# Kernel tuning notes

Measured on AMD Instinct MI355X. Metric: run time of the kernel, lower is better.

The kernel has to match this reference:

```python
import jax, jax.numpy as jnp
import numpy as np

B, S, H, I = 2, 2048, 4096, 11008  # batch, seq, hidden_size, intermediate_size (Llama-7B)


def setup_inputs() -> dict:
    key = jax.random.key(0)
    ks = jax.random.split(key, 11)
    # int8 activations and weights (SmoothQuant W8A8)
    hidden_states = jax.random.randint(ks[0], (B, S, H), -128, 128, dtype=jnp.int8)
    w_gate = jax.random.randint(ks[1], (I, H), -128, 128, dtype=jnp.int8)
    w_up = jax.random.randint(ks[2], (I, H), -128, 128, dtype=jnp.int8)
    w_down = jax.random.randint(ks[3], (H, I), -128, 128, dtype=jnp.int8)
    # dequant scales (alpha = input_scale * weight_scale), small positive
    gate_a = jax.random.uniform(ks[4], (1,), dtype=jnp.float32) * 1e-4 + 1e-5
    up_a = jax.random.uniform(ks[5], (1,), dtype=jnp.float32) * 1e-4 + 1e-5
    down_a = jax.random.uniform(ks[6], (1,), dtype=jnp.float32) * 1e-4 + 1e-5
    # fp32 biases
    gate_b = jax.random.normal(ks[7], (I,), dtype=jnp.float32) * 0.01
    up_b = jax.random.normal(ks[8], (I,), dtype=jnp.float32) * 0.01
    down_b = jax.random.normal(ks[9], (H,), dtype=jnp.float32) * 0.01
    # requantization scale for down_proj input
    down_scale = jax.random.uniform(ks[10], (1,), dtype=jnp.float32) * 0.05 + 0.01
    return {
        "hidden_states": hidden_states,
        "w_gate": w_gate, "w_up": w_up, "w_down": w_down,
        "gate_a": gate_a, "gate_b": gate_b,
        "up_a": up_a, "up_b": up_b,
        "down_a": down_a, "down_b": down_b,
        "down_scale": down_scale,
    }


def _i8_gemm(x_i8, w_i8):
    return jnp.einsum("bsk,nk->bsn", x_i8, w_i8, preferred_element_type=jnp.int32)


def reference(hidden_states, w_gate, w_up, w_down,
              gate_a, gate_b, up_a, up_b, down_a, down_b, down_scale):
    # gate_proj: W8A8 GEMM -> dequant (alpha) + fp32 bias -> fused SiLU
    g = _i8_gemm(hidden_states, w_gate).astype(jnp.float32) * gate_a[0] + gate_b
    gate_out = g * jax.nn.sigmoid(g)  # SiLU
    # up_proj: W8A8 GEMM -> dequant + fp32 bias
    up_out = _i8_gemm(hidden_states, w_up).astype(jnp.float32) * up_a[0] + up_b
    inter = gate_out * up_out
    # requantize to int8 for down_proj input
    q = jnp.clip(jnp.round(inter / down_scale[0]), -128, 127).astype(jnp.int8)
    # down_proj: W8A8 GEMM -> dequant + fp32 bias
    down_out = _i8_gemm(q, w_down).astype(jnp.float32) * down_a[0] + down_b
    return down_out  # [B, S, H] fp32
```

## Files before the change

kernel.cpp:

```cpp
#include <hip/hip_runtime.h>
#include <cstdint>


typedef int v4i  __attribute__((ext_vector_type(4)));
typedef int v16i __attribute__((ext_vector_type(16)));

typedef const void __attribute__((address_space(1)))* gas_ptr;
typedef void __attribute__((address_space(3)))* las_ptr;

static constexpr int M_TOT = 4096;
static constexpr int HDIM  = 4096;
static constexpr int IDIM  = 11008;

#define MFMA_I8(a, b, c) __builtin_amdgcn_mfma_i32_32x32x32_i8((a), (b), (c), 0, 0, 0)
#define BAR()        asm volatile("s_barrier" ::: "memory")
#define WAIT_VM(N)   asm volatile("s_waitcnt vmcnt(" #N ")" ::: "memory")
#define SETPRIO(P)   __builtin_amdgcn_s_setprio(P)

__device__ __forceinline__ void gload16(const int8_t* g, int8_t* l) {
  __builtin_amdgcn_global_load_lds((gas_ptr)g, (las_ptr)l, 16, 0, 0);
}

__device__ __forceinline__ v4i frag64(const int8_t* lds, int row, int c) {
  const int pair = row >> 1;
  const int slot = ((c << 1) | (row & 1)) ^ (pair & 7);
  return *(const v4i*)(lds + pair * 128 + slot * 16);
}

__device__ __forceinline__ void relmap64(int rel, int& row, int& col) {
  const int pair = rel >> 3;
  const int sl = (rel & 7) ^ (pair & 7);
  row = 2 * pair + (sl & 1);
  col = (sl >> 1) * 16;
}

__device__ __forceinline__ void pack16(const int* __restrict__ src,
                                       int8_t* __restrict__ dst, int t) {
  const int4* s = (const int4*)(src) + t * 4;
  int4 v0 = s[0], v1 = s[1], v2 = s[2], v3 = s[3];
  int p0 = (v0.x & 0xff) | ((v0.y & 0xff) << 8) | ((v0.z & 0xff) << 16) | (v0.w << 24);
  int p1 = (v1.x & 0xff) | ((v1.y & 0xff) << 8) | ((v1.z & 0xff) << 16) | (v1.w << 24);
  int p2 = (v2.x & 0xff) | ((v2.y & 0xff) << 8) | ((v2.z & 0xff) << 16) | (v2.w << 24);
  int p3 = (v3.x & 0xff) | ((v3.y & 0xff) << 8) | ((v3.z & 0xff) << 16) | (v3.w << 24);
  ((int4*)dst)[t] = make_int4(p0, p1, p2, p3);
}

static constexpr int CX = (M_TOT * HDIM) / 16;
static constexpr int CW = (IDIM * HDIM) / 16;
static constexpr int CTOT = CX + 3 * CW;

__global__ __launch_bounds__(256) void k_pack_all(
    const int* __restrict__ X32, const int* __restrict__ Wg32,
    const int* __restrict__ Wu32, const int* __restrict__ Wd32,
    int8_t* __restrict__ Xp, int8_t* __restrict__ Wgp,
    int8_t* __restrict__ Wup, int8_t* __restrict__ Wdp) {
  int t = blockIdx.x * blockDim.x + threadIdx.x;
  if (t >= CTOT) return;
  if (t < CX)               { pack16(X32,  Xp,  t); return; }
  t -= CX;
  if (t < CW)               { pack16(Wg32, Wgp, t); return; }
  t -= CW;
  if (t < CW)               { pack16(Wu32, Wup, t); return; }
  t -= CW;
  pack16(Wd32, Wdp, t);
}

__global__ __launch_bounds__(256, 2) void k_gateup(
    const int8_t* __restrict__ X,
    const int8_t* __restrict__ Wg,
    const int8_t* __restrict__ Wu,
    const float* __restrict__ gate_a, const float* __restrict__ gate_b,
    const float* __restrict__ up_a,   const float* __restrict__ up_b,
    const float* __restrict__ down_scale,
    int8_t* __restrict__ Q) {
  __shared__ __align__(16) int8_t lds8[3 * 24576];

  const int tid  = threadIdx.x;
  const int lane = tid & 63;
  const int wave = tid >> 6;
  const int wn   = wave;
  const int half = lane >> 5;
  const int ln31 = lane & 31;

  const int m0 = blockIdx.x * 128;
  const int n0 = blockIdx.y * 128;

  const int8_t* Ab = X  + (size_t)m0 * HDIM;
  const int8_t* Gb = Wg + (size_t)n0 * HDIM;
  const int8_t* Ub = Wu + (size_t)n0 * HDIM;

  int r0, c0, r1, c1;
  relmap64(tid,       r0, c0);
  relmap64(tid + 256, r1, c1);
  const size_t o0 = (size_t)r0 * HDIM + c0;
  const size_t o1 = (size_t)r1 * HDIM + c1;
  const int l0 = tid * 16;
  const int l1 = (tid + 256) * 16;

  v16i accG[4], accU[4];
#pragma unroll
  for (int i = 0; i < 4; ++i)
#pragma unroll
    for (int e = 0; e < 16; ++e) { accG[i][e] = 0; accU[i][e] = 0; }

  const int rB = wn * 32 + ln31;

#define GU_STAGE(rr, bb)                                        \
  {                                                             \
    int8_t* sb = &lds8[(bb) * 24576];                           \
    const size_t ks = (size_t)(rr) * 64;                        \
    gload16(Ab + ks + o0, sb + l0);                             \
    gload16(Ab + ks + o1, sb + l1);                             \
    gload16(Gb + ks + o0, sb + 8192 + l0);                      \
    gload16(Gb + ks + o1, sb + 8192 + l1);                      \
    gload16(Ub + ks + o0, sb + 16384 + l0);                     \
    gload16(Ub + ks + o1, sb + 16384 + l1);                     \
  }

  GU_STAGE(0, 0)
  GU_STAGE(1, 1)
  WAIT_VM(6);
  BAR();

  const int NT = HDIM / 64;
  int bc = 0;
  int bs = 2;
  for (int r = 0; r < NT; ++r) {
    if (r + 2 < NT) GU_STAGE(r + 2, bs)

    const int8_t* bufA = &lds8[bc * 24576];
    const int8_t* bufG = bufA + 8192;
    const int8_t* bufU = bufA + 16384;
    SETPRIO(1);
#pragma unroll
    for (int ks = 0; ks < 2; ++ks) {
      const int c = 2 * ks + half;
      v4i a0 = frag64(bufA, ln31,      c);
      v4i a1 = frag64(bufA, ln31 + 32, c);
      v4i a2 = frag64(bufA, ln31 + 64, c);
      v4i a3 = frag64(bufA, ln31 + 96, c);
      v4i gg = frag64(bufG, rB, c);
      v4i uu = frag64(bufU, rB, c);
      accG[0] = MFMA_I8(a0, gg, accG[0]);
      accU[0] = MFMA_I8(a0, uu, accU[0]);
      accG[1] = MFMA_I8(a1, gg, accG[1]);
      accU[1] = MFMA_I8(a1, uu, accU[1]);
      accG[2] = MFMA_I8(a2, gg, accG[2]);
      accU[2] = MFMA_I8(a2, uu, accU[2]);
      accG[3] = MFMA_I8(a3, gg, accG[3]);
      accU[3] = MFMA_I8(a3, uu, accU[3]);
    }
    SETPRIO(0);

    if (r + 2 < NT)      { WAIT_VM(6); }
    else if (r + 1 < NT) { WAIT_VM(0); }
    if (r + 1 < NT) BAR();

    bc = (bc == 2) ? 0 : bc + 1;
    bs = (bs == 2) ? 0 : bs + 1;
  }
#undef GU_STAGE

  const float ga = gate_a[0];
  const float ua = up_a[0];
  const float inv_ds = 1.0f / down_scale[0];
  const int n = n0 + wn * 32 + ln31;
  const float gb = gate_b[n];
  const float ub = up_b[n];

#pragma unroll
  for (int tm = 0; tm < 4; ++tm) {
#pragma unroll
    for (int r = 0; r < 16; ++r) {
      const int row_l = (r & 3) + 8 * (r >> 2) + 4 * half;
      const int m = m0 + tm * 32 + row_l;
      const float g = (float)accG[tm][r] * ga + gb;
      const float u = (float)accU[tm][r] * ua + ub;
      const float sg = g / (1.0f + __expf(-g));
      const float inter = sg * u;
      float qf = rintf(inter * inv_ds);
      qf = fminf(127.0f, fmaxf(-128.0f, qf));
      Q[(size_t)m * IDIM + n] = (int8_t)qf;
    }
  }
}

__global__ __launch_bounds__(256, 2) void k_down(
    const int8_t* __restrict__ Qm,
    const int8_t* __restrict__ Wd,
    const float* __restrict__ down_a, const float* __restrict__ down_b,
    float* __restrict__ Out) {
  __shared__ __align__(16) int8_t lds8[3 * 24576];

  const int tid  = threadIdx.x;
  const int lane = tid & 63;
  const int wave = tid >> 6;
  const int wn   = wave;
  const int half = lane >> 5;
  const int ln31 = lane & 31;

  const int m0 = blockIdx.x * 128;
  const int n0 = blockIdx.y * 256;

  const int8_t* Ab = Qm + (size_t)m0 * IDIM;
  const int8_t* Bb = Wd + (size_t)n0 * IDIM;

  int ra0, ca0, ra1, ca1;
  relmap64(tid,       ra0, ca0);
  relmap64(tid + 256, ra1, ca1);
  const size_t oa0 = (size_t)ra0 * IDIM + ca0;
  const size_t oa1 = (size_t)ra1 * IDIM + ca1;
  int rb0, cb0, rb1, cb1, rb2, cb2, rb3, cb3;
  relmap64(tid,       rb0, cb0);
  relmap64(tid + 256, rb1, cb1);
  relmap64(tid + 512, rb2, cb2);
  relmap64(tid + 768, rb3, cb3);
  const size_t ob0 = (size_t)rb0 * IDIM + cb0;
  const size_t ob1 = (size_t)rb1 * IDIM + cb1;
  const size_t ob2 = (size_t)rb2 * IDIM + cb2;
  const size_t ob3 = (size_t)rb3 * IDIM + cb3;
  const int l0 = tid * 16;
  const int l1 = (tid + 256) * 16;
  const int l2 = (tid + 512) * 16;
  const int l3 = (tid + 768) * 16;

  v16i acc[4][2];
#pragma unroll
  for (int i = 0; i < 4; ++i)
#pragma unroll
    for (int j = 0; j < 2; ++j)
#pragma unroll
      for (int e = 0; e < 16; ++e) acc[i][j][e] = 0;

  const int rB = wn * 64 + ln31;

#define DN_STAGE(rr, bb)                                        \
  {                                                             \
    int8_t* sb = &lds8[(bb) * 24576];                           \
    const size_t ks = (size_t)(rr) * 64;                        \
    gload16(Ab + ks + oa0, sb + l0);                            \
    gload16(Ab + ks + oa1, sb + l1);                            \
    gload16(Bb + ks + ob0, sb + 8192 + l0);                     \
    gload16(Bb + ks + ob1, sb + 8192 + l1);                     \
    gload16(Bb + ks + ob2, sb + 8192 + l2);                     \
    gload16(Bb + ks + ob3, sb + 8192 + l3);                     \
  }

  DN_STAGE(0, 0)
  DN_STAGE(1, 1)
  WAIT_VM(6);
  BAR();

  const int NT = IDIM / 64;
  int bc = 0;
  int bs = 2;
  for (int r = 0; r < NT; ++r) {
    if (r + 2 < NT) DN_STAGE(r + 2, bs)

    const int8_t* bufA = &lds8[bc * 24576];
    const int8_t* bufB = bufA + 8192;
    SETPRIO(1);
#pragma unroll
    for (int ks = 0; ks < 2; ++ks) {
      const int c = 2 * ks + half;
      v4i a0 = frag64(bufA, ln31,      c);
      v4i a1 = frag64(bufA, ln31 + 32, c);
      v4i a2 = frag64(bufA, ln31 + 64, c);
      v4i a3 = frag64(bufA, ln31 + 96, c);
      v4i b0 = frag64(bufB, rB,      c);
      v4i b1 = frag64(bufB, rB + 32, c);
      acc[0][0] = MFMA_I8(a0, b0, acc[0][0]);
      acc[0][1] = MFMA_I8(a0, b1, acc[0][1]);
      acc[1][0] = MFMA_I8(a1, b0, acc[1][0]);
      acc[1][1] = MFMA_I8(a1, b1, acc[1][1]);
      acc[2][0] = MFMA_I8(a2, b0, acc[2][0]);
      acc[2][1] = MFMA_I8(a2, b1, acc[2][1]);
      acc[3][0] = MFMA_I8(a3, b0, acc[3][0]);
      acc[3][1] = MFMA_I8(a3, b1, acc[3][1]);
    }
    SETPRIO(0);

    if (r + 2 < NT)      { WAIT_VM(6); }
    else if (r + 1 < NT) { WAIT_VM(0); }
    if (r + 1 < NT) BAR();

    bc = (bc == 2) ? 0 : bc + 1;
    bs = (bs == 2) ? 0 : bs + 1;
  }
#undef DN_STAGE

  const float da = down_a[0];
#pragma unroll
  for (int tn = 0; tn < 2; ++tn) {
    const int n = n0 + wn * 64 + tn * 32 + ln31;
    const float db = down_b[n];
#pragma unroll
    for (int tm = 0; tm < 4; ++tm) {
#pragma unroll
      for (int r = 0; r < 16; ++r) {
        const int row_l = (r & 3) + 8 * (r >> 2) + 4 * half;
        const int m = m0 + tm * 32 + row_l;
        Out[(size_t)m * HDIM + n] = (float)acc[tm][tn][r] * da + db;
      }
    }
  }
}

extern "C" void kernel_launch(void* const* d_in, const int* in_sizes, int n_in,
                              void* d_out, int out_size, void* d_ws, size_t ws_size,
                              hipStream_t stream) {
  const int* X32        = (const int*)d_in[0];
  const int* Wg32       = (const int*)d_in[1];
  const int* Wu32       = (const int*)d_in[2];
  const int* Wd32       = (const int*)d_in[3];
  const float* gate_a   = (const float*)d_in[4];
  const float* gate_b   = (const float*)d_in[5];
  const float* up_a     = (const float*)d_in[6];
  const float* up_b     = (const float*)d_in[7];
  const float* down_a   = (const float*)d_in[8];
  const float* down_b   = (const float*)d_in[9];
  const float* down_scale = (const float*)d_in[10];
  float* Out = (float*)d_out;

  const size_t nX = (size_t)M_TOT * HDIM;
  const size_t nW = (size_t)IDIM * HDIM;

  int8_t* Q   = (int8_t*)d_ws;
  int8_t* Xp  = Q   + nW;
  int8_t* Wgp = Xp  + nX;
  int8_t* Wup = Wgp + nW;
  int8_t* Wdp = Wup + nW;

  k_pack_all<<<(CTOT + 255) / 256, 256, 0, stream>>>(X32, Wg32, Wu32, Wd32,
                                                     Xp, Wgp, Wup, Wdp);

  k_gateup<<<dim3(M_TOT / 128, IDIM / 128), dim3(256), 0, stream>>>(
      Xp, Wgp, Wup, gate_a, gate_b, up_a, up_b, down_scale, Q);

  k_down<<<dim3(M_TOT / 128, HDIM / 256), dim3(256), 0, stream>>>(
      Q, Wdp, down_a, down_b, Out);
}
```

Measured before the change: 1.143 ms.

## Load weight fragments directly to registers and stage only activations in LDS

Both GEMM kernels stop staging the weight tiles through LDS. Each lane now loads its B fragments straight from global memory into registers, double-buffered across iterations. Only the activation tile is staged in LDS, with the K step widened to 128 and three buffers kept. The aim is to cut LDS traffic and footprint, at the cost of uncoalesced 16-byte strided global loads per lane, more registers, and intricate vmcnt bookkeeping.

```diff
diff --git a/kernel.cpp b/kernel.cpp
--- a/kernel.cpp
+++ b/kernel.cpp
@@ -21,10 +21,11 @@
   __builtin_amdgcn_global_load_lds((gas_ptr)g, (las_ptr)l, 16, 0, 0);
 }
 
-__device__ __forceinline__ v4i frag64(const int8_t* lds, int row, int c) {
+__device__ __forceinline__ v4i fragA(const int8_t* buf, int row, int cg) {
   const int pair = row >> 1;
+  const int c    = cg & 3;
   const int slot = ((c << 1) | (row & 1)) ^ (pair & 7);
-  return *(const v4i*)(lds + pair * 128 + slot * 16);
+  return *(const v4i*)(buf + (cg >> 2) * 8192 + pair * 128 + slot * 16);
 }
 
 __device__ __forceinline__ void relmap64(int rel, int& row, int& col) {
@@ -33,6 +34,8 @@
   row = 2 * pair + (sl & 1);
   col = (sl >> 1) * 16;
 }
+
+__device__ __forceinline__ int inc3(int b) { return b == 2 ? 0 : b + 1; }
 
 __device__ __forceinline__ void pack16(const int* __restrict__ src,
                                        int8_t* __restrict__ dst, int t) {
@@ -65,6 +68,45 @@
   pack16(Wd32, Wdp, t);
 }
 
+__device__ __forceinline__ void stage_a(const int8_t* Ab, size_t ldk, int rr,
+                                        size_t o0, size_t o1, int l0, int l1,
+                                        int8_t* base) {
+  const int8_t* g = Ab + (size_t)rr * 128;
+  gload16(g + o0,      base + l0);
+  gload16(g + o1,      base + l1);
+  gload16(g + 64 + o0, base + 8192 + l0);
+  gload16(g + 64 + o1, base + 8192 + l1);
+  (void)ldk;
+}
+
+__device__ __forceinline__ void loadB_row(const int8_t* p, v4i (&b)[4]) {
+#pragma unroll
+  for (int i = 0; i < 4; ++i) b[i] = *(const v4i*)(p + i * 32);
+}
+
+__device__ __forceinline__ void gu_compute(const int8_t* buf, int ln31, int half,
+                                           const v4i (&bg)[4], const v4i (&bu)[4],
+                                           v16i (&accG)[4], v16i (&accU)[4]) {
+  SETPRIO(1);
+#pragma unroll
+  for (int ks = 0; ks < 4; ++ks) {
+    const int cg = 2 * ks + half;
+    v4i a0 = fragA(buf, ln31,      cg);
+    v4i a1 = fragA(buf, ln31 + 32, cg);
+    v4i a2 = fragA(buf, ln31 + 64, cg);
+    v4i a3 = fragA(buf, ln31 + 96, cg);
+    accG[0] = MFMA_I8(a0, bg[ks], accG[0]);
+    accU[0] = MFMA_I8(a0, bu[ks], accU[0]);
+    accG[1] = MFMA_I8(a1, bg[ks], accG[1]);
+    accU[1] = MFMA_I8(a1, bu[ks], accU[1]);
+    accG[2] = MFMA_I8(a2, bg[ks], accG[2]);
+    accU[2] = MFMA_I8(a2, bu[ks], accU[2]);
+    accG[3] = MFMA_I8(a3, bg[ks], accG[3]);
+    accU[3] = MFMA_I8(a3, bu[ks], accU[3]);
+  }
+  SETPRIO(0);
+}
+
 __global__ __launch_bounds__(256, 2) void k_gateup(
     const int8_t* __restrict__ X,
     const int8_t* __restrict__ Wg,
@@ -73,93 +115,83 @@
     const float* __restrict__ up_a,   const float* __restrict__ up_b,
     const float* __restrict__ down_scale,
     int8_t* __restrict__ Q) {
-  __shared__ __align__(16) int8_t lds8[3 * 24576];
+  __shared__ __align__(16) int8_t lds8[3 * 16384];
 
   const int tid  = threadIdx.x;
   const int lane = tid & 63;
-  const int wave = tid >> 6;
-  const int wn   = wave;
+  const int wn   = tid >> 6;
   const int half = lane >> 5;
   const int ln31 = lane & 31;
 
   const int m0 = blockIdx.x * 128;
   const int n0 = blockIdx.y * 128;
 
-  const int8_t* Ab = X  + (size_t)m0 * HDIM;
-  const int8_t* Gb = Wg + (size_t)n0 * HDIM;
-  const int8_t* Ub = Wu + (size_t)n0 * HDIM;
+  const int8_t* Ab = X + (size_t)m0 * HDIM;
 
   int r0, c0, r1, c1;
   relmap64(tid,       r0, c0);
   relmap64(tid + 256, r1, c1);
-  const size_t o0 = (size_t)r0 * HDIM + c0;
-  const size_t o1 = (size_t)r1 * HDIM + c1;
+  const size_t oA0 = (size_t)r0 * HDIM + c0;
+  const size_t oA1 = (size_t)r1 * HDIM + c1;
   const int l0 = tid * 16;
   const int l1 = (tid + 256) * 16;
 
+  const int n_lane = n0 + wn * 32 + ln31;
+  const int8_t* Gp = Wg + (size_t)n_lane * HDIM + half * 16;
+  const int8_t* Up = Wu + (size_t)n_lane * HDIM + half * 16;
+
   v16i accG[4], accU[4];
 #pragma unroll
   for (int i = 0; i < 4; ++i)
 #pragma unroll
     for (int e = 0; e < 16; ++e) { accG[i][e] = 0; accU[i][e] = 0; }
 
-  const int rB = wn * 32 + ln31;
-
-#define GU_STAGE(rr, bb)                                        \
-  {                                                             \
-    int8_t* sb = &lds8[(bb) * 24576];                           \
-    const size_t ks = (size_t)(rr) * 64;                        \
-    gload16(Ab + ks + o0, sb + l0);                             \
-    gload16(Ab + ks + o1, sb + l1);                             \
-    gload16(Gb + ks + o0, sb + 8192 + l0);                      \
-    gload16(Gb + ks + o1, sb + 8192 + l1);                      \
-    gload16(Ub + ks + o0, sb + 16384 + l0);                     \
-    gload16(Ub + ks + o1, sb + 16384 + l1);                     \
-  }
-
-  GU_STAGE(0, 0)
-  GU_STAGE(1, 1)
-  WAIT_VM(6);
+  v4i bG0[4], bU0[4], bG1[4], bU1[4];
+
+  const int NT = HDIM / 128;
+
+  stage_a(Ab, HDIM, 0, oA0, oA1, l0, l1, lds8);
+  stage_a(Ab, HDIM, 1, oA0, oA1, l0, l1, lds8 + 16384);
+  loadB_row(Gp, bG0);
+  loadB_row(Up, bU0);
+  WAIT_VM(12);
   BAR();
 
-  const int NT = HDIM / 64;
-  int bc = 0;
-  int bs = 2;
-  for (int r = 0; r < NT; ++r) {
-    if (r + 2 < NT) GU_STAGE(r + 2, bs)
-
-    const int8_t* bufA = &lds8[bc * 24576];
-    const int8_t* bufG = bufA + 8192;
-    const int8_t* bufU = bufA + 16384;
-    SETPRIO(1);
-#pragma unroll
-    for (int ks = 0; ks < 2; ++ks) {
-      const int c = 2 * ks + half;
-      v4i a0 = frag64(bufA, ln31,      c);
-      v4i a1 = frag64(bufA, ln31 + 32, c);
-      v4i a2 = frag64(bufA, ln31 + 64, c);
-      v4i a3 = frag64(bufA, ln31 + 96, c);
-      v4i gg = frag64(bufG, rB, c);
-      v4i uu = frag64(bufU, rB, c);
-      accG[0] = MFMA_I8(a0, gg, accG[0]);
-      accU[0] = MFMA_I8(a0, uu, accU[0]);
-      accG[1] = MFMA_I8(a1, gg, accG[1]);
-      accU[1] = MFMA_I8(a1, uu, accU[1]);
-      accG[2] = MFMA_I8(a2, gg, accG[2]);
-      accU[2] = MFMA_I8(a2, uu, accU[2]);
-      accG[3] = MFMA_I8(a3, gg, accG[3]);
-      accU[3] = MFMA_I8(a3, uu, accU[3]);
-    }
-    SETPRIO(0);
-
-    if (r + 2 < NT)      { WAIT_VM(6); }
-    else if (r + 1 < NT) { WAIT_VM(0); }
-    if (r + 1 < NT) BAR();
-
-    bc = (bc == 2) ? 0 : bc + 1;
-    bs = (bs == 2) ? 0 : bs + 1;
-  }
-#undef GU_STAGE
+  int bcur = 0;
+  for (int r = 0; r < NT; r += 2) {
+    {
+      if (r + 1 < NT) {
+        loadB_row(Gp + (size_t)(r + 1) * 128, bG1);
+        loadB_row(Up + (size_t)(r + 1) * 128, bU1);
+      }
+      if (r + 2 < NT) {
+        const int bst = inc3(inc3(bcur));
+        stage_a(Ab, HDIM, r + 2, oA0, oA1, l0, l1, lds8 + bst * 16384);
+      }
+      gu_compute(lds8 + bcur * 16384, ln31, half, bG0, bU0, accG, accU);
+      if (r + 1 < NT) {
+        if (r + 2 < NT) { WAIT_VM(12); } else { WAIT_VM(8); }
+        BAR();
+      }
+      bcur = inc3(bcur);
+    }
+    {
+      if (r + 2 < NT) {
+        loadB_row(Gp + (size_t)(r + 2) * 128, bG0);
+        loadB_row(Up + (size_t)(r + 2) * 128, bU0);
+      }
+      if (r + 3 < NT) {
+        const int bst = inc3(inc3(bcur));
+        stage_a(Ab, HDIM, r + 3, oA0, oA1, l0, l1, lds8 + bst * 16384);
+      }
+      gu_compute(lds8 + bcur * 16384, ln31, half, bG1, bU1, accG, accU);
+      if (r + 2 < NT) {
+        if (r + 3 < NT) { WAIT_VM(12); } else { WAIT_VM(8); }
+        BAR();
+      }
+      bcur = inc3(bcur);
+    }
+  }
 
   const float ga = gate_a[0];
   const float ua = up_a[0];
@@ -171,11 +203,11 @@
 #pragma unroll
   for (int tm = 0; tm < 4; ++tm) {
 #pragma unroll
-    for (int r = 0; r < 16; ++r) {
-      const int row_l = (r & 3) + 8 * (r >> 2) + 4 * half;
+    for (int e = 0; e < 16; ++e) {
+      const int row_l = (e & 3) + 8 * (e >> 2) + 4 * half;
       const int m = m0 + tm * 32 + row_l;
-      const float g = (float)accG[tm][r] * ga + gb;
-      const float u = (float)accU[tm][r] * ua + ub;
+      const float g = (float)accG[tm][e] * ga + gb;
+      const float u = (float)accU[tm][e] * ua + ub;
       const float sg = g / (1.0f + __expf(-g));
       const float inter = sg * u;
       float qf = rintf(inter * inv_ds);
@@ -185,17 +217,39 @@
   }
 }
 
+__device__ __forceinline__ void dn_compute(const int8_t* buf, int ln31, int half,
+                                           const v4i (&b0)[4], const v4i (&b1)[4],
+                                           v16i (&acc)[4][2]) {
+  SETPRIO(1);
+#pragma unroll
+  for (int ks = 0; ks < 4; ++ks) {
+    const int cg = 2 * ks + half;
+    v4i a0 = fragA(buf, ln31,      cg);
+    v4i a1 = fragA(buf, ln31 + 32, cg);
+    v4i a2 = fragA(buf, ln31 + 64, cg);
+    v4i a3 = fragA(buf, ln31 + 96, cg);
+    acc[0][0] = MFMA_I8(a0, b0[ks], acc[0][0]);
+    acc[0][1] = MFMA_I8(a0, b1[ks], acc[0][1]);
+    acc[1][0] = MFMA_I8(a1, b0[ks], acc[1][0]);
+    acc[1][1] = MFMA_I8(a1, b1[ks], acc[1][1]);
+    acc[2][0] = MFMA_I8(a2, b0[ks], acc[2][0]);
+    acc[2][1] = MFMA_I8(a2, b1[ks], acc[2][1]);
+    acc[3][0] = MFMA_I8(a3, b0[ks], acc[3][0]);
+    acc[3][1] = MFMA_I8(a3, b1[ks], acc[3][1]);
+  }
+  SETPRIO(0);
+}
+
 __global__ __launch_bounds__(256, 2) void k_down(
     const int8_t* __restrict__ Qm,
     const int8_t* __restrict__ Wd,
     const float* __restrict__ down_a, const float* __restrict__ down_b,
     float* __restrict__ Out) {
-  __shared__ __align__(16) int8_t lds8[3 * 24576];
+  __shared__ __align__(16) int8_t lds8[3 * 16384];
 
   const int tid  = threadIdx.x;
   const int lane = tid & 63;
-  const int wave = tid >> 6;
-  const int wn   = wave;
+  const int wn   = tid >> 6;
   const int half = lane >> 5;
   const int ln31 = lane & 31;
 
@@ -203,26 +257,18 @@
   const int n0 = blockIdx.y * 256;
 
   const int8_t* Ab = Qm + (size_t)m0 * IDIM;
-  const int8_t* Bb = Wd + (size_t)n0 * IDIM;
-
-  int ra0, ca0, ra1, ca1;
-  relmap64(tid,       ra0, ca0);
-  relmap64(tid + 256, ra1, ca1);
-  const size_t oa0 = (size_t)ra0 * IDIM + ca0;
-  const size_t oa1 = (size_t)ra1 * IDIM + ca1;
-  int rb0, cb0, rb1, cb1, rb2, cb2, rb3, cb3;
-  relmap64(tid,       rb0, cb0);
-  relmap64(tid + 256, rb1, cb1);
-  relmap64(tid + 512, rb2, cb2);
-  relmap64(tid + 768, rb3, cb3);
-  const size_t ob0 = (size_t)rb0 * IDIM + cb0;
-  const size_t ob1 = (size_t)rb1 * IDIM + cb1;
-  const size_t ob2 = (size_t)rb2 * IDIM + cb2;
-  const size_t ob3 = (size_t)rb3 * IDIM + cb3;
+
+  int r0, c0, r1, c1;
+  relmap64(tid,       r0, c0);
+  relmap64(tid + 256, r1, c1);
+  const size_t oA0 = (size_t)r0 * IDIM + c0;
+  const size_t oA1 = (size_t)r1 * IDIM + c1;
   const int l0 = tid * 16;
   const int l1 = (tid + 256) * 16;
-  const int l2 = (tid + 512) * 16;
-  const int l3 = (tid + 768) * 16;
+
+  const int n_row0 = n0 + wn * 64 + ln31;
+  const int8_t* B0p = Wd + (size_t)n_row0 * IDIM + half * 16;
+  const int8_t* B1p = B0p + (size_t)32 * IDIM;
 
   v16i acc[4][2];
 #pragma unroll
@@ -232,62 +278,52 @@
 #pragma unroll
       for (int e = 0; e < 16; ++e) acc[i][j][e] = 0;
 
-  const int rB = wn * 64 + ln31;
-
-#define DN_STAGE(rr, bb)                                        \
-  {                                                             \
-    int8_t* sb = &lds8[(bb) * 24576];                           \
-    const size_t ks = (size_t)(rr) * 64;                        \
-    gload16(Ab + ks + oa0, sb + l0);                            \
-    gload16(Ab + ks + oa1, sb + l1);                            \
-    gload16(Bb + ks + ob0, sb + 8192 + l0);                     \
-    gload16(Bb + ks + ob1, sb + 8192 + l1);                     \
-    gload16(Bb + ks + ob2, sb + 8192 + l2);                     \
-    gload16(Bb + ks + ob3, sb + 8192 + l3);                     \
-  }
-
-  DN_STAGE(0, 0)
-  DN_STAGE(1, 1)
-  WAIT_VM(6);
+  v4i bA0[4], bB0[4], bA1[4], bB1[4];
+
+  const int NT = IDIM / 128;
+
+  stage_a(Ab, IDIM, 0, oA0, oA1, l0, l1, lds8);
+  stage_a(Ab, IDIM, 1, oA0, oA1, l0, l1, lds8 + 16384);
+  loadB_row(B0p, bA0);
+  loadB_row(B1p, bB0);
+  WAIT_VM(12);
   BAR();
 
-  const int NT = IDIM / 64;
-  int bc = 0;
-  int bs = 2;
-  for (int r = 0; r < NT; ++r) {
-    if (r + 2 < NT) DN_STAGE(r + 2, bs)
-
-    const int8_t* bufA = &lds8[bc * 24576];
-    const int8_t* bufB = bufA + 8192;
-    SETPRIO(1);
-#pragma unroll
-    for (int ks = 0; ks < 2; ++ks) {
-      const int c = 2 * ks + half;
-      v4i a0 = frag64(bufA, ln31,      c);
-      v4i a1 = frag64(bufA, ln31 + 32, c);
-      v4i a2 = frag64(bufA, ln31 + 64, c);
-      v4i a3 = frag64(bufA, ln31 + 96, c);
-      v4i b0 = frag64(bufB, rB,      c);
-      v4i b1 = frag64(bufB, rB + 32, c);
-      acc[0][0] = MFMA_I8(a0, b0, acc[0][0]);
-      acc[0][1] = MFMA_I8(a0, b1, acc[0][1]);
-      acc[1][0] = MFMA_I8(a1, b0, acc[1][0]);
-      acc[1][1] = MFMA_I8(a1, b1, acc[1][1]);
-      acc[2][0] = MFMA_I8(a2, b0, acc[2][0]);
-      acc[2][1] = MFMA_I8(a2, b1, acc[2][1]);
-      acc[3][0] = MFMA_I8(a3, b0, acc[3][0]);
-      acc[3][1] = MFMA_I8(a3, b1, acc[3][1]);
-    }
-    SETPRIO(0);
-
-    if (r + 2 < NT)      { WAIT_VM(6); }
-    else if (r + 1 < NT) { WAIT_VM(0); }
-    if (r + 1 < NT) BAR();
-
-    bc = (bc == 2) ? 0 : bc + 1;
-    bs = (bs == 2) ? 0 : bs + 1;
-  }
-#undef DN_STAGE
+  int bcur = 0;
+  for (int r = 0; r < NT; r += 2) {
+    {
+      if (r + 1 < NT) {
+        loadB_row(B0p + (size_t)(r + 1) * 128, bA1);
+        loadB_row(B1p + (size_t)(r + 1) * 128, bB1);
+      }
+      if (r + 2 < NT) {
+        const int bst = inc3(inc3(bcur));
+        stage_a(Ab, IDIM, r + 2, oA0, oA1, l0, l1, lds8 + bst * 16384);
+      }
+      dn_compute(lds8 + bcur * 16384, ln31, half, bA0, bB0, acc);
+      if (r + 1 < NT) {
+        if (r + 2 < NT) { WAIT_VM(12); } else { WAIT_VM(8); }
+        BAR();
+      }
+      bcur = inc3(bcur);
+    }
+    {
+      if (r + 2 < NT) {
+        loadB_row(B0p + (size_t)(r + 2) * 128, bA0);
+        loadB_row(B1p + (size_t)(r + 2) * 128, bB0);
+      }
+      if (r + 3 < NT) {
+        const int bst = inc3(inc3(bcur));
+        stage_a(Ab, IDIM, r + 3, oA0, oA1, l0, l1, lds8 + bst * 16384);
+      }
+      dn_compute(lds8 + bcur * 16384, ln31, half, bA1, bB1, acc);
+      if (r + 2 < NT) {
+        if (r + 3 < NT) { WAIT_VM(12); } else { WAIT_VM(8); }
+        BAR();
+      }
+      bcur = inc3(bcur);
+    }
+  }
 
   const float da = down_a[0];
 #pragma unroll
@@ -297,10 +333,10 @@
 #pragma unroll
     for (int tm = 0; tm < 4; ++tm) {
 #pragma unroll
-      for (int r = 0; r < 16; ++r) {
-        const int row_l = (r & 3) + 8 * (r >> 2) + 4 * half;
+      for (int e = 0; e < 16; ++e) {
+        const int row_l = (e & 3) + 8 * (e >> 2) + 4 * half;
         const int m = m0 + tm * 32 + row_l;
-        Out[(size_t)m * HDIM + n] = (float)acc[tm][tn][r] * da + db;
+        Out[(size_t)m * HDIM + n] = (float)acc[tm][tn][e] * da + db;
       }
     }
   }
```

After: 1.246 ms. +9.0%, slower.
